# Performance work log

Measured on AMD Instinct MI355X. Metric: run time of the kernel, lower is better.

## Reference

```python
import jax, jax.numpy as jnp
import numpy as np

COS_EPS = 0.001
THRESHOLD = 0.1
LEAKY_SLOPE = 0.01


def setup_inputs() -> dict:
    key = jax.random.key(0)
    k1, k2 = jax.random.split(key)
    B, N, D_in, D_out = 4, 4096, 256, 128
    b_het_z = jax.random.normal(k1, (B, N, D_in), dtype=jnp.float32)
    # xavier_uniform with gain=1.414
    gain = 1.414
    bound = gain * np.sqrt(6.0 / (D_in + D_out))
    W = jax.random.uniform(k2, (D_in, D_out), dtype=jnp.float32, minval=-bound, maxval=bound)
    return {"b_het_z": b_het_z, "W": W}


def reference(b_het_z, W):
    # h: [B, N, D_out]
    h = jnp.matmul(b_het_z, W)
    h = jax.nn.leaky_relu(h, negative_slope=LEAKY_SLOPE)
    # pairwise cosine similarity via normalized GEMM (avoids O(N^2*D) broadcast)
    # torch CosineSimilarity: dot(x, y) / max(||x|| * ||y||, eps)
    norms = jnp.linalg.norm(h, axis=-1)  # [B, N]
    dots = jnp.einsum("bnd,bmd->bnm", h, h)  # [B, N, N]
    denom = jnp.maximum(norms[:, :, None] * norms[:, None, :], COS_EPS)
    b_adj = jnp.abs(dots / denom)
    # nn.Threshold(t, 0): keep x if x > t else 0
    b_adj = jnp.where(b_adj > THRESHOLD, b_adj, 0.0)
    return b_adj
```

## Files before the change

kernel.cpp:

```cpp
#include <hip/hip_runtime.h>
#include <math.h>

#define NTOK 4096
#define RTOT 16384
#define DIN  256
#define DOUT 128

constexpr float LEAKY = 0.01f;
constexpr float CEPS  = 0.001f;
constexpr float THR   = 0.1f;

__global__ __launch_bounds__(256, 2) void proj_kernel(
    const float* __restrict__ A, const float* __restrict__ W,
    float* __restrict__ H, float* __restrict__ norms)
{
    __shared__ float As[32 * DIN];
    __shared__ float Ws[64 * DOUT];
    const int tid  = threadIdx.x;
    const int row0 = blockIdx.x * 32;

    {
        const float4* src = (const float4*)(A + (size_t)row0 * DIN);
        float4* dst = (float4*)As;
        #pragma unroll
        for (int it = 0; it < 8; ++it)
            dst[tid + it * 256] = src[tid + it * 256];
    }

    const int tx = tid & 31;
    const int ty = tid >> 5;

    float acc[4][4];
    #pragma unroll
    for (int i = 0; i < 4; ++i)
        #pragma unroll
        for (int j = 0; j < 4; ++j) acc[i][j] = 0.f;

    for (int kc = 0; kc < DIN; kc += 64) {
        __syncthreads();
        {
            const float4* wsrc = (const float4*)(W + (size_t)kc * DOUT);
            float4* wdst = (float4*)Ws;
            #pragma unroll
            for (int it = 0; it < 8; ++it)
                wdst[tid + it * 256] = wsrc[tid + it * 256];
        }
        __syncthreads();

        for (int k = 0; k < 64; k += 4) {
            float4 w4[4];
            #pragma unroll
            for (int s = 0; s < 4; ++s)
                w4[s] = *(const float4*)(Ws + (k + s) * DOUT + 4 * tx);
            #pragma unroll
            for (int i = 0; i < 4; ++i) {
                float4 a4 = *(const float4*)(As + (ty + 8 * i) * DIN + kc + k);
                float ak[4] = {a4.x, a4.y, a4.z, a4.w};
                #pragma unroll
                for (int s = 0; s < 4; ++s) {
                    float wj[4] = {w4[s].x, w4[s].y, w4[s].z, w4[s].w};
                    #pragma unroll
                    for (int j = 0; j < 4; ++j)
                        acc[i][j] = fmaf(ak[s], wj[j], acc[i][j]);
                }
            }
        }
    }

    #pragma unroll
    for (int i = 0; i < 4; ++i) {
        float h[4];
        float s = 0.f;
        #pragma unroll
        for (int j = 0; j < 4; ++j) {
            float v = acc[i][j];
            h[j] = (v >= 0.f) ? v : LEAKY * v;
            s = fmaf(h[j], h[j], s);
        }
        float4 hv = {h[0], h[1], h[2], h[3]};
        const int r = row0 + ty + 8 * i;
        *(float4*)(H + (size_t)r * DOUT + 4 * tx) = hv;
        #pragma unroll
        for (int m = 16; m >= 1; m >>= 1)
            s += __shfl_xor(s, m, 64);
        if (tx == 0) norms[r] = sqrtf(s);
    }
}

#define TILE 128
#define NT   (NTOK / TILE)
#define NPAIR (NT * (NT + 1) / 2)
#define KC   32
#define LDA  36
#define LDB  132

__global__ __launch_bounds__(256, 4) void cos_kernel(
    const float* __restrict__ H, const float* __restrict__ norms,
    float* __restrict__ out)
{
    __shared__ float smem[TILE * LDA + KC * LDB];
    float* As = smem;
    float* Bs = smem + TILE * LDA;

    const int b = blockIdx.y;
    const int p = blockIdx.x;
    int bj = (int)((sqrtf(8.f * (float)p + 1.f) - 1.f) * 0.5f);
    while ((bj + 1) * (bj + 2) / 2 <= p) ++bj;
    while (bj * (bj + 1) / 2 > p) --bj;
    const int bi = p - bj * (bj + 1) / 2;
    const int ti = bi * TILE;
    const int tj = bj * TILE;

    const int tid  = threadIdx.x;
    const int wave = tid >> 6;
    const int lane = tid & 63;
    const int qr = wave & 1;
    const int qc = wave >> 1;
    const int tx = lane & 7;
    const int ty = lane >> 3;
    const float* Hb = H + (size_t)b * NTOK * DOUT;

    float4 acc4[8][2];
    #pragma unroll
    for (int i = 0; i < 8; ++i)
        #pragma unroll
        for (int jv = 0; jv < 2; ++jv)
            acc4[i][jv] = make_float4(0.f, 0.f, 0.f, 0.f);

    const int sr = tid >> 3;
    const int sk = (tid & 7) << 2;

    for (int kc = 0; kc < DOUT; kc += KC) {
        __syncthreads();
        #pragma unroll
        for (int it = 0; it < 4; ++it) {
            const int r = sr + it * 32;
            *(float4*)(As + r * LDA + sk) =
                *(const float4*)(Hb + (size_t)(ti + r) * DOUT + kc + sk);
            float4 v = *(const float4*)(Hb + (size_t)(tj + r) * DOUT + kc + sk);
            Bs[(sk + 0) * LDB + r] = v.x;
            Bs[(sk + 1) * LDB + r] = v.y;
            Bs[(sk + 2) * LDB + r] = v.z;
            Bs[(sk + 3) * LDB + r] = v.w;
        }
        __syncthreads();

        #pragma unroll
        for (int k = 0; k < KC; k += 4) {
            float4 af[8];
            #pragma unroll
            for (int i = 0; i < 8; ++i)
                af[i] = *(const float4*)(As + (qr * 64 + ty + 8 * i) * LDA + k);
            #pragma unroll
            for (int kk = 0; kk < 4; ++kk) {
                const float* brow = Bs + (k + kk) * LDB + qc * 64 + 4 * tx;
                float4 b0 = *(const float4*)(brow);
                float4 b1 = *(const float4*)(brow + 32);
                #pragma unroll
                for (int i = 0; i < 8; ++i) {
                    const float a = ((const float*)&af[i])[kk];
                    acc4[i][0].x = fmaf(a, b0.x, acc4[i][0].x);
                    acc4[i][0].y = fmaf(a, b0.y, acc4[i][0].y);
                    acc4[i][0].z = fmaf(a, b0.z, acc4[i][0].z);
                    acc4[i][0].w = fmaf(a, b0.w, acc4[i][0].w);
                    acc4[i][1].x = fmaf(a, b1.x, acc4[i][1].x);
                    acc4[i][1].y = fmaf(a, b1.y, acc4[i][1].y);
                    acc4[i][1].z = fmaf(a, b1.z, acc4[i][1].z);
                    acc4[i][1].w = fmaf(a, b1.w, acc4[i][1].w);
                }
            }
        }
    }

    float rn[8];
    float4 cn[2];
    #pragma unroll
    for (int i = 0; i < 8; ++i)
        rn[i] = norms[b * NTOK + ti + qr * 64 + ty + 8 * i];
    #pragma unroll
    for (int jv = 0; jv < 2; ++jv) {
        const int c = tj + qc * 64 + 32 * jv + 4 * tx;
        cn[jv] = make_float4(norms[b * NTOK + c],     norms[b * NTOK + c + 1],
                             norms[b * NTOK + c + 2], norms[b * NTOK + c + 3]);
    }
    #pragma unroll
    for (int i = 0; i < 8; ++i)
        #pragma unroll
        for (int jv = 0; jv < 2; ++jv) {
            float* a = (float*)&acc4[i][jv];
            const float* n = (const float*)&cn[jv];
            #pragma unroll
            for (int s = 0; s < 4; ++s) {
                float denom = fmaxf(rn[i] * n[s], CEPS);
                float v = fabsf(a[s] / denom);
                a[s] = (v > THR) ? v : 0.f;
            }
        }

    float* Ob = out + (size_t)b * NTOK * NTOK;

    #pragma unroll
    for (int i = 0; i < 8; ++i) {
        const size_t rowbase = (size_t)(ti + qr * 64 + ty + 8 * i) * NTOK + tj;
        #pragma unroll
        for (int jv = 0; jv < 2; ++jv)
            *(float4*)(Ob + rowbase + qc * 64 + 32 * jv + 4 * tx) = acc4[i][jv];
    }

    if (bi != bj) {
        float* T = smem;
        #pragma unroll
        for (int h = 0; h < 2; ++h) {
            __syncthreads();
            if (qc == h) {
                #pragma unroll
                for (int jv = 0; jv < 2; ++jv) {
                    const int c0 = 32 * jv + 4 * tx;
                    #pragma unroll
                    for (int i = 0; i < 8; ++i) {
                        const int r = qr * 64 + ty + 8 * i;
                        const float* a = (const float*)&acc4[i][jv];
                        T[(c0 + 0) * LDB + r] = a[0];
                        T[(c0 + 1) * LDB + r] = a[1];
                        T[(c0 + 2) * LDB + r] = a[2];
                        T[(c0 + 3) * LDB + r] = a[3];
                    }
                }
            }
            __syncthreads();
            #pragma unroll
            for (int it = 0; it < 8; ++it) {
                const int idx = tid + it * 256;
                const int rt  = idx >> 5;
                const int c4  = (idx & 31) << 2;
                *(float4*)(Ob + (size_t)(tj + 64 * h + rt) * NTOK + ti + c4) =
                    *(const float4*)(T + rt * LDB + c4);
            }
        }
    }
}

extern "C" void kernel_launch(void* const* d_in, const int* in_sizes, int n_in,
                              void* d_out, int out_size, void* d_ws, size_t ws_size,
                              hipStream_t stream) {
    const float* A = (const float*)d_in[0];
    const float* W = (const float*)d_in[1];
    float* out = (float*)d_out;

    float* Hws   = (float*)d_ws;
    float* norms = Hws + (size_t)RTOT * DOUT;

    proj_kernel<<<RTOT / 32, 256, 0, stream>>>(A, W, Hws, norms);
    cos_kernel<<<dim3(NPAIR, 4), 256, 0, stream>>>(Hws, norms, out);
}
```

Measured before the change: 405.9 us.

## Use split-bf16 MFMA on pre-normalized rows for cosine GEMM

The projection kernel now normalizes each row by its inverse norm and stores it as a bf16 hi/lo pair. The cosine kernel computes the Gram tile with three bf16 32x32x16 MFMAs per step (hi*hi, hi*lo, lo*hi), which replaces the FP32 FMA loop. Symmetric tiling and the transposed store are dropped, so every 128x128 tile is computed on its own and the per-element division is gone. This trades roughly twice the tile compute for tensor-core throughput. The epilogue now writes scalar stores strided across rows, which may coalesce poorly. The eps clamp is gone, so a zero-norm row would give NaN.

```diff
diff --git a/kernel.cpp b/kernel.cpp
--- a/kernel.cpp
+++ b/kernel.cpp
@@ -7,12 +7,23 @@
 #define DOUT 128
 
 constexpr float LEAKY = 0.01f;
-constexpr float CEPS  = 0.001f;
 constexpr float THR   = 0.1f;
+
+typedef __attribute__((ext_vector_type(8)))  short bf16x8;
+typedef __attribute__((ext_vector_type(16))) float f32x16;
+
+__device__ __forceinline__ unsigned short f2bf(float x) {
+    unsigned u = __float_as_uint(x);
+    unsigned r = (u + 0x7fffu + ((u >> 16) & 1u)) >> 16;
+    return (unsigned short)r;
+}
+__device__ __forceinline__ float bf2f(unsigned short h) {
+    return __uint_as_float((unsigned)h << 16);
+}
 
 __global__ __launch_bounds__(256, 2) void proj_kernel(
     const float* __restrict__ A, const float* __restrict__ W,
-    float* __restrict__ H, float* __restrict__ norms)
+    unsigned short* __restrict__ Hhi, unsigned short* __restrict__ Hlo)
 {
     __shared__ float As[32 * DIN];
     __shared__ float Ws[64 * DOUT];
@@ -77,164 +88,121 @@
             h[j] = (v >= 0.f) ? v : LEAKY * v;
             s = fmaf(h[j], h[j], s);
         }
-        float4 hv = {h[0], h[1], h[2], h[3]};
-        const int r = row0 + ty + 8 * i;
-        *(float4*)(H + (size_t)r * DOUT + 4 * tx) = hv;
         #pragma unroll
         for (int m = 16; m >= 1; m >>= 1)
             s += __shfl_xor(s, m, 64);
-        if (tx == 0) norms[r] = sqrtf(s);
-    }
-}
-
-#define TILE 128
-#define NT   (NTOK / TILE)
-#define NPAIR (NT * (NT + 1) / 2)
-#define KC   32
-#define LDA  36
-#define LDB  132
+        const float rinv = 1.0f / sqrtf(s);
+        const int r = row0 + ty + 8 * i;
+        ushort4 hv, lv;
+        {
+            float n0 = h[0] * rinv; hv.x = f2bf(n0); lv.x = f2bf(n0 - bf2f(hv.x));
+            float n1 = h[1] * rinv; hv.y = f2bf(n1); lv.y = f2bf(n1 - bf2f(hv.y));
+            float n2 = h[2] * rinv; hv.z = f2bf(n2); lv.z = f2bf(n2 - bf2f(hv.z));
+            float n3 = h[3] * rinv; hv.w = f2bf(n3); lv.w = f2bf(n3 - bf2f(hv.w));
+        }
+        *(ushort4*)(Hhi + (size_t)r * DOUT + 4 * tx) = hv;
+        *(ushort4*)(Hlo + (size_t)r * DOUT + 4 * tx) = lv;
+    }
+}
 
 __global__ __launch_bounds__(256, 4) void cos_kernel(
-    const float* __restrict__ H, const float* __restrict__ norms,
+    const unsigned short* __restrict__ Hhi,
+    const unsigned short* __restrict__ Hlo,
     float* __restrict__ out)
 {
-    __shared__ float smem[TILE * LDA + KC * LDB];
-    float* As = smem;
-    float* Bs = smem + TILE * LDA;
-
-    const int b = blockIdx.y;
-    const int p = blockIdx.x;
-    int bj = (int)((sqrtf(8.f * (float)p + 1.f) - 1.f) * 0.5f);
-    while ((bj + 1) * (bj + 2) / 2 <= p) ++bj;
-    while (bj * (bj + 1) / 2 > p) --bj;
-    const int bi = p - bj * (bj + 1) / 2;
-    const int ti = bi * TILE;
-    const int tj = bj * TILE;
+    __shared__ uint4 smem4[2048];
+    char* smem = (char*)smem4;
+
+    const int b  = blockIdx.y;
+    const int ti = (blockIdx.x >> 5) << 7;
+    const int tj = (blockIdx.x & 31) << 7;
+    const int bN = b * NTOK;
 
     const int tid  = threadIdx.x;
     const int wave = tid >> 6;
     const int lane = tid & 63;
     const int qr = wave & 1;
     const int qc = wave >> 1;
-    const int tx = lane & 7;
-    const int ty = lane >> 3;
-    const float* Hb = H + (size_t)b * NTOK * DOUT;
-
-    float4 acc4[8][2];
-    #pragma unroll
-    for (int i = 0; i < 8; ++i)
-        #pragma unroll
-        for (int jv = 0; jv < 2; ++jv)
-            acc4[i][jv] = make_float4(0.f, 0.f, 0.f, 0.f);
-
-    const int sr = tid >> 3;
-    const int sk = (tid & 7) << 2;
-
-    for (int kc = 0; kc < DOUT; kc += KC) {
-        __syncthreads();
-        #pragma unroll
-        for (int it = 0; it < 4; ++it) {
-            const int r = sr + it * 32;
-            *(float4*)(As + r * LDA + sk) =
-                *(const float4*)(Hb + (size_t)(ti + r) * DOUT + kc + sk);
-            float4 v = *(const float4*)(Hb + (size_t)(tj + r) * DOUT + kc + sk);
-            Bs[(sk + 0) * LDB + r] = v.x;
-            Bs[(sk + 1) * LDB + r] = v.y;
-            Bs[(sk + 2) * LDB + r] = v.z;
-            Bs[(sk + 3) * LDB + r] = v.w;
-        }
-        __syncthreads();
-
-        #pragma unroll
-        for (int k = 0; k < KC; k += 4) {
-            float4 af[8];
-            #pragma unroll
-            for (int i = 0; i < 8; ++i)
-                af[i] = *(const float4*)(As + (qr * 64 + ty + 8 * i) * LDA + k);
-            #pragma unroll
-            for (int kk = 0; kk < 4; ++kk) {
-                const float* brow = Bs + (k + kk) * LDB + qc * 64 + 4 * tx;
-                float4 b0 = *(const float4*)(brow);
-                float4 b1 = *(const float4*)(brow + 32);
+    const int lr = lane & 31;
+    const int hh = lane >> 5;
+
+    f32x16 acc[2][2];
+    #pragma unroll
+    for (int i = 0; i < 2; ++i)
+        #pragma unroll
+        for (int j = 0; j < 2; ++j)
+            #pragma unroll
+            for (int e = 0; e < 16; ++e)
+                acc[i][j][e] = 0.f;
+
+    for (int kc = 0; kc < DOUT; kc += 32) {
+        __syncthreads();
+        #pragma unroll
+        for (int half = 0; half < 2; ++half) {
+            uint4 v[4];
+            int   d[4];
+            #pragma unroll
+            for (int q = 0; q < 4; ++q) {
+                const int u  = (half * 4 + q) * 256 + tid;
+                const int m  = u >> 9;
+                const int w  = u & 511;
+                const int r  = w >> 2;
+                const int sl = w & 3;
+                const unsigned short* src = (m & 1) ? Hlo : Hhi;
+                const int rb = (m < 2) ? ti : tj;
+                v[q] = *(const uint4*)(src + (((size_t)(bN + rb + r)) << 7)
+                                           + kc + (sl << 3));
+                d[q] = (m << 13) + (r << 6) + ((sl ^ (r & 3)) << 4);
+            }
+            #pragma unroll
+            for (int q = 0; q < 4; ++q)
+                *(uint4*)(smem + d[q]) = v[q];
+        }
+        __syncthreads();
+
+        #pragma unroll
+        for (int ks = 0; ks < 2; ++ks) {
+            bf16x8 ah[2], al[2], bh[2], bl[2];
+            const int s = (ks << 1) | hh;
+            #pragma unroll
+            for (int t = 0; t < 2; ++t) {
+                const int ra = qr * 64 + t * 32 + lr;
+                const int oa = (ra << 6) + ((s ^ (ra & 3)) << 4);
+                ah[t] = *(const bf16x8*)(smem + oa);
+                al[t] = *(const bf16x8*)(smem + 8192 + oa);
+                const int rb = qc * 64 + t * 32 + lr;
+                const int ob = (rb << 6) + ((s ^ (rb & 3)) << 4);
+                bh[t] = *(const bf16x8*)(smem + 16384 + ob);
+                bl[t] = *(const bf16x8*)(smem + 24576 + ob);
+            }
+            #pragma unroll
+            for (int i = 0; i < 2; ++i)
                 #pragma unroll
-                for (int i = 0; i < 8; ++i) {
-                    const float a = ((const float*)&af[i])[kk];
-                    acc4[i][0].x = fmaf(a, b0.x, acc4[i][0].x);
-                    acc4[i][0].y = fmaf(a, b0.y, acc4[i][0].y);
-                    acc4[i][0].z = fmaf(a, b0.z, acc4[i][0].z);
-                    acc4[i][0].w = fmaf(a, b0.w, acc4[i][0].w);
-                    acc4[i][1].x = fmaf(a, b1.x, acc4[i][1].x);
-                    acc4[i][1].y = fmaf(a, b1.y, acc4[i][1].y);
-                    acc4[i][1].z = fmaf(a, b1.z, acc4[i][1].z);
-                    acc4[i][1].w = fmaf(a, b1.w, acc4[i][1].w);
+                for (int j = 0; j < 2; ++j) {
+                    acc[i][j] = __builtin_amdgcn_mfma_f32_32x32x16_bf16(
+                                    ah[i], bh[j], acc[i][j], 0, 0, 0);
+                    acc[i][j] = __builtin_amdgcn_mfma_f32_32x32x16_bf16(
+                                    ah[i], bl[j], acc[i][j], 0, 0, 0);
+                    acc[i][j] = __builtin_amdgcn_mfma_f32_32x32x16_bf16(
+                                    al[i], bh[j], acc[i][j], 0, 0, 0);
                 }
-            }
-        }
-    }
-
-    float rn[8];
-    float4 cn[2];
-    #pragma unroll
-    for (int i = 0; i < 8; ++i)
-        rn[i] = norms[b * NTOK + ti + qr * 64 + ty + 8 * i];
-    #pragma unroll
-    for (int jv = 0; jv < 2; ++jv) {
-        const int c = tj + qc * 64 + 32 * jv + 4 * tx;
-        cn[jv] = make_float4(norms[b * NTOK + c],     norms[b * NTOK + c + 1],
-                             norms[b * NTOK + c + 2], norms[b * NTOK + c + 3]);
-    }
-    #pragma unroll
-    for (int i = 0; i < 8; ++i)
-        #pragma unroll
-        for (int jv = 0; jv < 2; ++jv) {
-            float* a = (float*)&acc4[i][jv];
-            const float* n = (const float*)&cn[jv];
-            #pragma unroll
-            for (int s = 0; s < 4; ++s) {
-                float denom = fmaxf(rn[i] * n[s], CEPS);
-                float v = fabsf(a[s] / denom);
-                a[s] = (v > THR) ? v : 0.f;
-            }
-        }
+        }
+    }
 
     float* Ob = out + (size_t)b * NTOK * NTOK;
-
-    #pragma unroll
-    for (int i = 0; i < 8; ++i) {
-        const size_t rowbase = (size_t)(ti + qr * 64 + ty + 8 * i) * NTOK + tj;
-        #pragma unroll
-        for (int jv = 0; jv < 2; ++jv)
-            *(float4*)(Ob + rowbase + qc * 64 + 32 * jv + 4 * tx) = acc4[i][jv];
-    }
-
-    if (bi != bj) {
-        float* T = smem;
-        #pragma unroll
-        for (int h = 0; h < 2; ++h) {
-            __syncthreads();
-            if (qc == h) {
-                #pragma unroll
-                for (int jv = 0; jv < 2; ++jv) {
-                    const int c0 = 32 * jv + 4 * tx;
-                    #pragma unroll
-                    for (int i = 0; i < 8; ++i) {
-                        const int r = qr * 64 + ty + 8 * i;
-                        const float* a = (const float*)&acc4[i][jv];
-                        T[(c0 + 0) * LDB + r] = a[0];
-                        T[(c0 + 1) * LDB + r] = a[1];
-                        T[(c0 + 2) * LDB + r] = a[2];
-                        T[(c0 + 3) * LDB + r] = a[3];
-                    }
-                }
-            }
-            __syncthreads();
-            #pragma unroll
-            for (int it = 0; it < 8; ++it) {
-                const int idx = tid + it * 256;
-                const int rt  = idx >> 5;
-                const int c4  = (idx & 31) << 2;
-                *(float4*)(Ob + (size_t)(tj + 64 * h + rt) * NTOK + ti + c4) =
-                    *(const float4*)(T + rt * LDB + c4);
+    const int col = tj + qc * 64 + lr;
+    #pragma unroll
+    for (int i = 0; i < 2; ++i) {
+        const int rbase = ti + qr * 64 + i * 32 + (hh << 2);
+        #pragma unroll
+        for (int j = 0; j < 2; ++j) {
+            const int c = col + j * 32;
+            #pragma unroll
+            for (int v = 0; v < 16; ++v) {
+                const int row = rbase + (v & 3) + ((v >> 2) << 3);
+                float x = fabsf(acc[i][j][v]);
+                x = (x > THR) ? x : 0.f;
+                Ob[(size_t)row * NTOK + c] = x;
             }
         }
     }
@@ -247,9 +215,9 @@
     const float* W = (const float*)d_in[1];
     float* out = (float*)d_out;
 
-    float* Hws   = (float*)d_ws;
-    float* norms = Hws + (size_t)RTOT * DOUT;
-
-    proj_kernel<<<RTOT / 32, 256, 0, stream>>>(A, W, Hws, norms);
-    cos_kernel<<<dim3(NPAIR, 4), 256, 0, stream>>>(Hws, norms, out);
-}
+    unsigned short* Hhi = (unsigned short*)d_ws;
+    unsigned short* Hlo = Hhi + (size_t)RTOT * DOUT;
+
+    proj_kernel<<<RTOT / 32, 256, 0, stream>>>(A, W, Hhi, Hlo);
+    cos_kernel<<<dim3(1024, 4), 256, 0, stream>>>(Hhi, Hlo, out);
+}
```

Result: faster. 339.7 us (-16.3%).
